# Performance work log

Hardware: AMD Instinct MI355X
Metric: run time of the kernel (lower is better)

## Reference

```python
import jax, jax.numpy as jnp
import numpy as np

D_MODEL = 384
D_INNER = 768   # expand=2
D_STATE = 16
DT_RANK = 24    # ceil(d_model/16)
D_CONV = 4
VOCAB = 50257
AUDIO_DIM = 80
B, L_AUDIO, L_TEXT = 2, 1024, 1024


def _conv1d(x, w, b, pad_l, pad_r, groups=1):
    # x: [B, C, L], w: [O, I/groups, K]
    y = jax.lax.conv_general_dilated(
        x, w, window_strides=(1,), padding=[(pad_l, pad_r)],
        feature_group_count=groups, dimension_numbers=('NCH', 'OIH', 'NCH'))
    return y + b[None, :, None]


def _mamba(x, in_w, convw, convb, xproj_w, dt_w, dt_b, A_log, Dp, out_w):
    # x: [B, L, D_MODEL]
    Bn, L, _ = x.shape
    xz = x @ in_w.T                       # [B, L, 2*D_INNER]
    xi, z = jnp.split(xz, 2, axis=-1)
    # causal depthwise conv (torch pads d_conv-1 both sides then slices [:L])
    xi = _conv1d(xi.transpose(0, 2, 1), convw, convb, D_CONV - 1, 0, groups=D_INNER)
    xi = jax.nn.silu(xi.transpose(0, 2, 1))          # [B, L, D_INNER]
    xdbl = xi @ xproj_w.T                            # [B, L, DT_RANK+2*D_STATE]
    dt, Bm, Cm = jnp.split(xdbl, [DT_RANK, DT_RANK + D_STATE], axis=-1)
    dt = jax.nn.softplus(dt @ dt_w.T + dt_b)         # [B, L, D_INNER]
    A = -jnp.exp(A_log)                              # [D_INNER, D_STATE]
    dA = jnp.exp(dt[..., None] * A)                  # [B, L, D_INNER, D_STATE]
    dBu = dt[..., None] * Bm[:, :, None, :] * xi[..., None]

    def step(h, inputs):
        dA_t, dBu_t, C_t = inputs
        h = dA_t * h + dBu_t                         # [B, D_INNER, D_STATE]
        y = jnp.einsum('bdn,bn->bd', h, C_t)
        return h, y

    h0 = jnp.zeros((Bn, D_INNER, D_STATE), dtype=x.dtype)
    _, ys = jax.lax.scan(step, h0,
                         (dA.transpose(1, 0, 2, 3), dBu.transpose(1, 0, 2, 3), Cm.transpose(1, 0, 2)))
    y = ys.transpose(1, 0, 2) + xi * Dp              # D skip connection
    y = y * jax.nn.silu(z)                           # gate
    return y @ out_w.T                               # [B, L, D_MODEL]


def setup_inputs() -> dict:
    key = jax.random.key(0)
    ks = jax.random.split(key, 16)

    def rn(k, shape, s=0.02):
        return jax.random.normal(k, shape, jnp.float32) * s

    inp = {}
    inp['audio_features'] = jax.random.normal(ks[0], (B, AUDIO_DIM, L_AUDIO), jnp.float32)
    inp['text_tokens'] = jax.random.randint(ks[1], (B, L_TEXT), 0, VOCAB)
    inp['conv1_w'] = rn(ks[2], (D_MODEL // 2, AUDIO_DIM, 3))
    inp['conv1_b'] = jnp.zeros((D_MODEL // 2,), jnp.float32)
    inp['conv2_w'] = rn(ks[3], (D_MODEL, D_MODEL // 2, 3))
    inp['conv2_b'] = jnp.zeros((D_MODEL,), jnp.float32)
    inp['embed'] = rn(ks[4], (VOCAB, D_MODEL))

    def mamba_params(kbase):
        kk = jax.random.split(kbase, 6)
        A = jnp.tile(jnp.arange(1, D_STATE + 1, dtype=jnp.float32), (D_INNER, 1))
        return dict(in_w=rn(kk[0], (2 * D_INNER, D_MODEL)),
                    convw=rn(kk[1], (D_INNER, 1, D_CONV)),
                    convb=jnp.zeros((D_INNER,), jnp.float32),
                    xproj_w=rn(kk[2], (DT_RANK + 2 * D_STATE, D_INNER)),
                    dt_w=rn(kk[3], (D_INNER, DT_RANK)),
                    dt_b=rn(kk[4], (D_INNER,), 0.1),
                    A_log=jnp.log(A),
                    Dp=jnp.ones((D_INNER,), jnp.float32),
                    out_w=rn(kk[5], (D_MODEL, D_INNER)))

    for i, p in enumerate([mamba_params(ks[5]), mamba_params(ks[6])], 1):
        for n, v in p.items():
            inp[f'm{i}_{n}'] = v
    inp['proj_w'] = rn(ks[7], (VOCAB, D_MODEL))
    inp['proj_b'] = jnp.zeros((VOCAB,), jnp.float32)
    return inp


def reference(audio_features, text_tokens, conv1_w, conv1_b, conv2_w, conv2_b, embed,
              m1_in_w, m1_convw, m1_convb, m1_xproj_w, m1_dt_w, m1_dt_b, m1_A_log, m1_Dp, m1_out_w,
              m2_in_w, m2_convw, m2_convb, m2_xproj_w, m2_dt_w, m2_dt_b, m2_A_log, m2_Dp, m2_out_w,
              proj_w, proj_b):
    a = jax.nn.relu(_conv1d(audio_features, conv1_w, conv1_b, 1, 1))
    a = _conv1d(a, conv2_w, conv2_b, 1, 1)
    audio_emb = a.transpose(0, 2, 1)                 # [B, L_audio, D_MODEL]
    text_emb = embed[text_tokens]                    # [B, L_text, D_MODEL]
    x = jnp.concatenate([audio_emb, text_emb], axis=1)
    x = _mamba(x, m1_in_w, m1_convw, m1_convb, m1_xproj_w, m1_dt_w, m1_dt_b, m1_A_log, m1_Dp, m1_out_w)
    x = _mamba(x, m2_in_w, m2_convw, m2_convb, m2_xproj_w, m2_dt_w, m2_dt_b, m2_A_log, m2_Dp, m2_out_w)
    return x @ proj_w.T + proj_b                     # [B, L, VOCAB]
```

## Files before the change

### kernel.cpp

```cpp
#include <hip/hip_runtime.h>

typedef unsigned short u16;
typedef __attribute__((ext_vector_type(4))) float f4;
typedef __attribute__((ext_vector_type(4))) float f32x4;
typedef __attribute__((ext_vector_type(8))) short short8;
typedef __attribute__((ext_vector_type(4))) unsigned short u16x4;

#define DEV static __device__ __forceinline__

DEV u16 f2bf(float f) {
  unsigned u = __float_as_uint(f);
  u += 0x7fffu + ((u >> 16) & 1u);
  return (u16)(u >> 16);
}
DEV float siluf(float z) { return z / (1.f + __expf(-z)); }

DEV void gload16(const u16* g, const u16* l) {
  __builtin_amdgcn_global_load_lds(
      (const __attribute__((address_space(1))) unsigned int*)(unsigned long long)g,
      (__attribute__((address_space(3))) unsigned int*)(unsigned int)(unsigned long long)l,
      16, 0, 0);
}

struct CvtArgs {
  const float* src[7];
  u16* dst[7];
  int bstart[8];
  int nq[7];
};

DEV void cvt_plain(const float* __restrict__ s, u16* __restrict__ d, int q, int nq) {
  if (q < nq) {
    f4 v = ((const f4*)s)[q];
    u16x4 o;
#pragma unroll
    for (int e = 0; e < 4; ++e) o[e] = f2bf(v[e]);
    ((u16x4*)d)[q] = o;
  }
}

__global__ void k_cvtmulti(CvtArgs a) {
  int b = blockIdx.x;
  int i = 0;
#pragma unroll
  for (int j = 1; j < 7; ++j) i += (b >= a.bstart[j]);
#pragma unroll
  for (int j = 0; j < 7; ++j) {
    if (i == j)
      cvt_plain(a.src[j], a.dst[j], (b - a.bstart[j]) * 256 + threadIdx.x, a.nq[j]);
  }
}

__global__ void k_wtrans(const float* __restrict__ in, float* __restrict__ out, int O, int I) {
  int n = O * I * 3;
  for (int g = blockIdx.x * blockDim.x + threadIdx.x; g < n; g += gridDim.x * blockDim.x) {
    int o = g / (I * 3);
    int rem = g - o * (I * 3);
    out[rem * O + o] = in[g];
  }
}

__global__ __launch_bounds__(192) void k_conv1(const float* __restrict__ audio,
    const float* __restrict__ w1t, const float* __restrict__ b1, float* __restrict__ a1t) {
  __shared__ float s[80][18];
  int bx = blockIdx.x;
  int b = bx >> 6, l0 = (bx & 63) << 4;
  int tid = threadIdx.x;
  for (int i = tid; i < 80 * 18; i += 192) {
    int ci = i / 18, dl = i - ci * 18;
    int l = l0 + dl - 1;
    s[ci][dl] = (l >= 0 && l < 1024) ? audio[(b * 80 + ci) * 1024 + l] : 0.f;
  }
  __syncthreads();
  int co = tid;
  float acc[16];
  float bias = b1[co];
#pragma unroll
  for (int i = 0; i < 16; ++i) acc[i] = bias;
  for (int ci = 0; ci < 80; ++ci) {
#pragma unroll
    for (int j = 0; j < 3; ++j) {
      float w = w1t[(ci * 3 + j) * 192 + co];
#pragma unroll
      for (int ls = 0; ls < 16; ++ls) acc[ls] = fmaf(s[ci][ls + j], w, acc[ls]);
    }
  }
#pragma unroll
  for (int ls = 0; ls < 16; ++ls) {
    float v = acc[ls] > 0.f ? acc[ls] : 0.f;
    a1t[(b * 1024 + l0 + ls) * 192 + co] = v;
  }
}

__global__ __launch_bounds__(384) void k_conv2b(const float* __restrict__ a1t,
    const float* __restrict__ w2t, const float* __restrict__ b2, u16* __restrict__ Xb) {
  __shared__ float s[10][192];
  int bx = blockIdx.x;
  int b = bx >> 7, l0 = (bx & 127) << 3;
  int tid = threadIdx.x;
  for (int i = tid; i < 10 * 192; i += 384) {
    int dl = i / 192, ci = i - dl * 192;
    int l = l0 + dl - 1;
    s[dl][ci] = (l >= 0 && l < 1024) ? a1t[(b * 1024 + l) * 192 + ci] : 0.f;
  }
  __syncthreads();
  int co = tid;
  float acc[8];
  float bias = b2[co];
#pragma unroll
  for (int i = 0; i < 8; ++i) acc[i] = bias;
  for (int ci = 0; ci < 192; ++ci) {
#pragma unroll
    for (int j = 0; j < 3; ++j) {
      float w = w2t[(ci * 3 + j) * 384 + co];
#pragma unroll
      for (int ls = 0; ls < 8; ++ls) acc[ls] = fmaf(s[ls + j][ci], w, acc[ls]);
    }
  }
#pragma unroll
  for (int ls = 0; ls < 8; ++ls)
    Xb[((size_t)(b * 2048 + l0 + ls)) * 384 + co] = f2bf(acc[ls]);
}

__global__ void k_embedb(const int* __restrict__ tok, const float* __restrict__ emb,
                         u16* __restrict__ Xb) {
  int gid = blockIdx.x * blockDim.x + threadIdx.x;
  if (gid >= 2 * 1024 * 96) return;
  int q = gid % 96;
  int rt = gid / 96;
  int b = rt >> 10, t = rt & 1023;
  int tk = tok[b * 1024 + t];
  f4 v = *(const f4*)(emb + (size_t)tk * 384 + q * 4);
  u16x4 o;
#pragma unroll
  for (int e = 0; e < 4; ++e) o[e] = f2bf(v[e]);
  *(u16x4*)(Xb + ((size_t)(b * 2048 + 1024 + t)) * 384 + q * 4) = o;
}

__global__ void k_dwconv2(const float* __restrict__ xz, const float* __restrict__ cw,
                          const float* __restrict__ cb, float* __restrict__ xif,
                          u16* __restrict__ xib) {
  int gid = blockIdx.x * blockDim.x + threadIdx.x;
  if (gid >= 4096 * 192) return;
  int d4 = gid % 192;
  int row = gid / 192;
  int b = row >> 11, l = row & 2047;
  int d = d4 * 4;
  f4 cw0 = *(const f4*)(cw + d * 4);
  f4 cw1 = *(const f4*)(cw + d * 4 + 4);
  f4 cw2 = *(const f4*)(cw + d * 4 + 8);
  f4 cw3 = *(const f4*)(cw + d * 4 + 12);
  f4 acc = *(const f4*)(cb + d);
#pragma unroll
  for (int j = 0; j < 4; ++j) {
    int lj = l - 3 + j;
    if (lj >= 0) {
      f4 v = *(const f4*)(xz + ((size_t)(b * 2048 + lj)) * 1536 + d);
      acc[0] = fmaf(v[0], cw0[j], acc[0]);
      acc[1] = fmaf(v[1], cw1[j], acc[1]);
      acc[2] = fmaf(v[2], cw2[j], acc[2]);
      acc[3] = fmaf(v[3], cw3[j], acc[3]);
    }
  }
  f4 o;
  u16x4 ob;
#pragma unroll
  for (int e = 0; e < 4; ++e) { o[e] = siluf(acc[e]); ob[e] = f2bf(o[e]); }
  *(f4*)(xif + (size_t)row * 768 + d) = o;
  *(u16x4*)(xib + (size_t)row * 768 + d) = ob;
}

template <int TILE, int BIAS, int ACT, int OUTB, int SWZ>
__global__ __launch_bounds__(256) void k_gemm2(
    const u16* __restrict__ A, int lda, const u16* __restrict__ W, int ldw,
    const float* __restrict__ bias, float* __restrict__ C, u16* __restrict__ Cb,
    int ldc, int M, int N, int K) {
  constexpr int MF = (TILE == 128) ? 4 : 2;
  constexpr int TB = TILE * 32;
  constexpr int NLD = (TILE == 128) ? 4 : 2;
  __shared__ u16 As[2][TB], Ws[2][TB];
  int bid = blockIdx.x;
  if (SWZ) {
    int nwg = gridDim.x;
    int q = nwg >> 3, r = nwg & 7;
    int xcd = bid & 7, li = bid >> 3;
    bid = (xcd < r ? xcd * (q + 1) : r * (q + 1) + (xcd - r) * q) + li;
  }
  int bm, bn;
  if (TILE == 128) { bm = (bid & 31) << 7; bn = (bid >> 5) << 7; }
  else             { bm = (bid & 63) << 6; bn = (bid >> 6) << 6; }
  int t = threadIdx.x, lane = t & 63, wave = t >> 6;
  int wm0, wn0;
  if (TILE == 128) { wm0 = (wave >> 1) << 6; wn0 = (wave & 1) << 6; }
  else             { wm0 = (wave >> 1) << 5; wn0 = (wave & 1) << 5; }
  int fr = lane & 15, fk = (lane >> 4) << 3;
  int r0 = t >> 2, sl = (t & 3) << 3;
  const u16* gA0 = A + (size_t)(bm + r0) * lda + sl;
  const u16* gA1 = gA0 + (size_t)64 * lda;
  int n0 = bn + r0;      if (n0 > N - 1) n0 = N - 1;
  int n1 = bn + r0 + 64; if (n1 > N - 1) n1 = N - 1;
  const u16* gW0 = W + (size_t)n0 * ldw + sl;
  const u16* gW1 = W + (size_t)n1 * ldw + sl;
  f32x4 acc[MF][MF] = {};
  int nk = K >> 5;
  auto stage = [&](int buf, int k0) {
    gload16(gA0 + k0, As[buf] + t * 8);
    gload16(gW0 + k0, Ws[buf] + t * 8);
    if (TILE == 128) {
      gload16(gA1 + k0, As[buf] + t * 8 + 2048);
      gload16(gW1 + k0, Ws[buf] + t * 8 + 2048);
    }
  };
  stage(0, 0);
  for (int s = 0; s < nk; ++s) {
    int cur = s & 1;
    if (s + 1 < nk) {
      stage(cur ^ 1, (s + 1) << 5);
      asm volatile("s_waitcnt vmcnt(%0)" :: "i"(NLD) : "memory");
    } else {
      asm volatile("s_waitcnt vmcnt(0)" ::: "memory");
    }
    __builtin_amdgcn_sched_barrier(0);
    __builtin_amdgcn_s_barrier();
    __builtin_amdgcn_sched_barrier(0);
    short8 af[MF], wf[MF];
#pragma unroll
    for (int mi = 0; mi < MF; ++mi) af[mi] = *(const short8*)&As[cur][(wm0 + mi * 16 + fr) * 32 + fk];
#pragma unroll
    for (int ni = 0; ni < MF; ++ni) wf[ni] = *(const short8*)&Ws[cur][(wn0 + ni * 16 + fr) * 32 + fk];
#pragma unroll
    for (int mi = 0; mi < MF; ++mi)
#pragma unroll
      for (int ni = 0; ni < MF; ++ni)
        acc[mi][ni] = __builtin_amdgcn_mfma_f32_16x16x32_bf16(af[mi], wf[ni], acc[mi][ni], 0, 0, 0);
    __builtin_amdgcn_sched_barrier(0);
    __builtin_amdgcn_s_barrier();
  }
  int frow = (lane >> 4) << 2;
#pragma unroll
  for (int ni = 0; ni < MF; ++ni) {
    int col = bn + wn0 + ni * 16 + fr;
    if (col < N) {
      float bv = BIAS ? bias[col] : 0.f;
#pragma unroll
      for (int mi = 0; mi < MF; ++mi) {
        int row = bm + wm0 + mi * 16 + frow;
#pragma unroll
        for (int rr = 0; rr < 4; ++rr) {
          float v = acc[mi][ni][rr] + bv;
          if (ACT == 1) v = (v > 20.f) ? v : log1pf(__expf(v));
          size_t o = (size_t)(row + rr) * ldc + col;
          if (OUTB == 0) C[o] = v;
          else if (OUTB == 1) Cb[o] = f2bf(v);
          else { C[o] = v; Cb[o] = f2bf(v); }
        }
      }
    }
  }
}

__global__ __launch_bounds__(256, 4) void k_gemmF(
    const u16* __restrict__ A, const u16* __restrict__ W,
    const float* __restrict__ bias, float* __restrict__ C,
    int ldc, int N) {
  __shared__ __align__(16) char smraw[40960];
  u16* As = (u16*)smraw;
  u16* Ws = (u16*)(smraw + 8192);
  float* Cs = (float*)smraw;
  int bid = blockIdx.x;
  {
    int nwg = gridDim.x;
    int q = nwg >> 3, r = nwg & 7;
    int xcd = bid & 7, li = bid >> 3;
    bid = (xcd < r ? xcd * (q + 1) : r * (q + 1) + (xcd - r) * q) + li;
  }
  int mg = bid / 1576;
  int rem = bid - mg * 1576;
  int np = rem >> 3, mi = rem & 7;
  int bm = ((mg << 3) + mi) << 6;
  int bn = np << 8;
  int t = threadIdx.x, lane = t & 63, wave = t >> 6;
  int wm0 = (wave >> 1) << 5;
  int wn0 = (wave & 1) << 7;
  int fr = lane & 15, hi = lane >> 4, fk = hi << 3;
  int r0 = t >> 2, sl = (t & 3) << 3;
  const u16* gA = A + (size_t)(bm + r0) * 384 + sl;
  int nrow[4];
#pragma unroll
  for (int i = 0; i < 4; ++i) {
    int gn = bn + r0 + i * 64;
    nrow[i] = (gn > N - 1) ? (N - 1) : gn;
  }
  const u16* gWs = W + sl;
  f32x4 acc[2][8] = {};
  auto stage = [&](int buf, int k0) {
    gload16(gA + k0, As + buf * 2048 + t * 8);
#pragma unroll
    for (int i = 0; i < 4; ++i)
      gload16(gWs + (size_t)nrow[i] * 384 + k0, Ws + buf * 8192 + t * 8 + i * 2048);
  };
  stage(0, 0);
  for (int s = 0; s < 12; ++s) {
    int cur = s & 1;
    if (s + 1 < 12) {
      stage(cur ^ 1, (s + 1) << 5);
      asm volatile("s_waitcnt vmcnt(5)" ::: "memory");
    } else {
      asm volatile("s_waitcnt vmcnt(0)" ::: "memory");
    }
    __builtin_amdgcn_sched_barrier(0);
    __builtin_amdgcn_s_barrier();
    __builtin_amdgcn_sched_barrier(0);
    short8 af[2];
#pragma unroll
    for (int mi2 = 0; mi2 < 2; ++mi2)
      af[mi2] = *(const short8*)&As[cur * 2048 + (wm0 + mi2 * 16 + fr) * 32 + fk];
#pragma unroll
    for (int ni = 0; ni < 8; ++ni) {
      short8 wf = *(const short8*)&Ws[cur * 8192 + (wn0 + ni * 16 + fr) * 32 + fk];
#pragma unroll
      for (int mi2 = 0; mi2 < 2; ++mi2)
        acc[mi2][ni] = __builtin_amdgcn_mfma_f32_16x16x32_bf16(af[mi2], wf, acc[mi2][ni], 0, 0, 0);
    }
    __builtin_amdgcn_sched_barrier(0);
    __builtin_amdgcn_s_barrier();
  }
  int cq = (t & 63) << 2;
  int gcol0 = bn + cq;
  f4 bv4;
  if (gcol0 + 3 < N) bv4 = *(const f4*)&bias[gcol0];
  else {
#pragma unroll
    for (int e = 0; e < 4; ++e) bv4[e] = (gcol0 + e < N) ? bias[gcol0 + e] : 0.f;
  }
  int frow = hi << 2;
#pragma unroll
  for (int c = 0; c < 2; ++c) {
    if (c) __syncthreads();
    if (wm0 == c * 32) {
#pragma unroll
      for (int ni = 0; ni < 8; ++ni) {
        int lc = wn0 + ni * 16 + fr;
#pragma unroll
        for (int mi2 = 0; mi2 < 2; ++mi2)
#pragma unroll
          for (int rr = 0; rr < 4; ++rr)
            Cs[(mi2 * 16 + frow + rr) * 260 + lc] = acc[mi2][ni][rr];
      }
    }
    __syncthreads();
#pragma unroll
    for (int p = 0; p < 8; ++p) {
      int lr = (p << 2) + (t >> 6);
      f4 v = *(const f4*)&Cs[lr * 260 + cq];
      v += bv4;
      float* cp = C + (size_t)(bm + c * 32 + lr) * ldc + gcol0;
      if (gcol0 + 3 < N) {
        __builtin_nontemporal_store(v, (f4*)cp);
      } else {
#pragma unroll
        for (int e = 0; e < 4; ++e)
          if (gcol0 + e < N) __builtin_nontemporal_store(v[e], cp + e);
      }
    }
  }
}

DEV int scan_ch0_w(int g, int w) { return (((g & 7) * 24) + ((g >> 3) << 2) + w) * 4; }

DEV void dt_inline(const float* __restrict__ xdbl, size_t rowbase, int lane,
                   const float* __restrict__ s_w, const float* __restrict__ s_b,
                   float (*s_dt)[4]) {
  const float* xr = xdbl + (rowbase + lane) * 56;
  f4 x0 = *(const f4*)xr,        x1 = *(const f4*)(xr + 4),  x2 = *(const f4*)(xr + 8);
  f4 x3 = *(const f4*)(xr + 12), x4 = *(const f4*)(xr + 16), x5 = *(const f4*)(xr + 20);
#pragma unroll
  for (int cc = 0; cc < 4; ++cc) {
    const float* w = s_w + cc * 24;
    float acc = s_b[cc];
#pragma unroll
    for (int q = 0; q < 4; ++q) acc = fmaf(x0[q], w[q], acc);
#pragma unroll
    for (int q = 0; q < 4; ++q) acc = fmaf(x1[q], w[4 + q], acc);
#pragma unroll
    for (int q = 0; q < 4; ++q) acc = fmaf(x2[q], w[8 + q], acc);
#pragma unroll
    for (int q = 0; q < 4; ++q) acc = fmaf(x3[q], w[12 + q], acc);
#pragma unroll
    for (int q = 0; q < 4; ++q) acc = fmaf(x4[q], w[16 + q], acc);
#pragma unroll
    for (int q = 0; q < 4; ++q) acc = fmaf(x5[q], w[20 + q], acc);
    s_dt[lane][cc] = (acc > 20.f) ? acc : log1pf(__expf(acc));
  }
}

__global__ __launch_bounds__(256) void k_scanA(
    const float* __restrict__ xdbl, const float* __restrict__ xi,
    const float* __restrict__ A_log,
    const float* __restrict__ dtw, const float* __restrict__ dtbias,
    float* __restrict__ Hloc, float* __restrict__ Sdt) {
  __shared__ float s_dt[4][64][4], s_w[4][96], s_b[4][4];
  int b = blockIdx.y, seg = blockIdx.z;
  int tid = threadIdx.x, w = tid >> 6, lane = tid & 63;
  int ch0 = scan_ch0_w(blockIdx.x, w);
  int c = lane >> 4, n = lane & 15;
  int d = ch0 + c;
  for (int i = lane; i < 96; i += 64) s_w[w][i] = dtw[ch0 * 24 + i];
  if (lane < 4) s_b[w][lane] = dtbias[ch0 + lane];
  size_t rowbase = (size_t)b * 2048 + seg * 64;
  __syncthreads();
  dt_inline(xdbl, rowbase, lane, s_w[w], s_b[w], s_dt[w]);
  __syncthreads();
  float a = -__expf(A_log[d * 16 + n]);
  float h = 0.f, sdt = 0.f;
  size_t row = rowbase;
#pragma unroll 4
  for (int i = 0; i < 64; ++i, ++row) {
    float dtv = s_dt[w][i][c];
    float xiv = xi[row * 768 + d];
    float Bv = xdbl[row * 56 + 24 + n];
    float da = __expf(dtv * a);
    h = fmaf(da, h, dtv * Bv * xiv);
    sdt += dtv;
  }
  size_t o = (((size_t)b * 32 + seg) * 768 + d) * 16 + n;
  Hloc[o] = h;
  if (n == 0) Sdt[((size_t)b * 32 + seg) * 768 + d] = sdt;
}

__global__ __launch_bounds__(256) void k_scanC(
    const float* __restrict__ xdbl, const float* __restrict__ xi,
    const float* __restrict__ xz, const float* __restrict__ A_log,
    const float* __restrict__ Dp,
    const float* __restrict__ dtw, const float* __restrict__ dtbias,
    const float* __restrict__ Hloc, const float* __restrict__ Sdt,
    u16* __restrict__ y) {
  __shared__ float s_dt[4][64][4], s_y[4][64][4], s_w[4][96], s_b[4][4];
  int b = blockIdx.y, seg = blockIdx.z;
  int tid = threadIdx.x, w = tid >> 6, lane = tid & 63;
  int ch0 = scan_ch0_w(blockIdx.x, w);
  int c = lane >> 4, n = lane & 15;
  int d = ch0 + c;
  for (int i = lane; i < 96; i += 64) s_w[w][i] = dtw[ch0 * 24 + i];
  if (lane < 4) s_b[w][lane] = dtbias[ch0 + lane];
  size_t rowbase = (size_t)b * 2048 + seg * 64;
  __syncthreads();
  dt_inline(xdbl, rowbase, lane, s_w[w], s_b[w], s_dt[w]);
  float a = -__expf(A_log[d * 16 + n]);
  float h = 0.f;
  for (int s = 0; s < seg; ++s) {
    float P = __expf(a * Sdt[((size_t)b * 32 + s) * 768 + d]);
    h = fmaf(P, h, Hloc[(((size_t)b * 32 + s) * 768 + d) * 16 + n]);
  }
  __syncthreads();
  size_t row = rowbase;
#pragma unroll 2
  for (int i = 0; i < 64; ++i, ++row) {
    float dtv = s_dt[w][i][c];
    float xiv = xi[row * 768 + d];
    float Bv = xdbl[row * 56 + 24 + n];
    float Cv = xdbl[row * 56 + 40 + n];
    float da = __expf(dtv * a);
    h = fmaf(da, h, dtv * Bv * xiv);
    float yv = h * Cv;
    yv += __shfl_xor(yv, 1);
    yv += __shfl_xor(yv, 2);
    yv += __shfl_xor(yv, 4);
    yv += __shfl_xor(yv, 8);
    if (n == 0) s_y[w][i][c] = yv;
  }
  __syncthreads();
  size_t rw = rowbase + lane;
  f4 xiv4 = *(const f4*)(xi + rw * 768 + ch0);
  f4 dpv = *(const f4*)(Dp + ch0);
  f4 zv = *(const f4*)(xz + rw * 1536 + 768 + ch0);
  u16x4 ob;
#pragma unroll
  for (int e = 0; e < 4; ++e) {
    float o = (s_y[w][lane][e] + xiv4[e] * dpv[e]) * siluf(zv[e]);
    ob[e] = f2bf(o);
  }
  *(u16x4*)(y + rw * 768 + ch0) = ob;
}

extern "C" void kernel_launch(void* const* d_in, const int* in_sizes, int n_in,
                              void* d_out, int out_size, void* d_ws, size_t ws_size,
                              hipStream_t stream) {
  const float* audio   = (const float*)d_in[0];
  const int*   tokens  = (const int*)d_in[1];
  const float* conv1_w = (const float*)d_in[2];
  const float* conv1_b = (const float*)d_in[3];
  const float* conv2_w = (const float*)d_in[4];
  const float* conv2_b = (const float*)d_in[5];
  const float* embedw  = (const float*)d_in[6];
  const float* P1[9], *P2[9];
  for (int i = 0; i < 9; ++i) { P1[i] = (const float*)d_in[7 + i]; P2[i] = (const float*)d_in[16 + i]; }
  const float* proj_w = (const float*)d_in[25];
  const float* proj_b = (const float*)d_in[26];
  (void)in_sizes; (void)n_in; (void)out_size; (void)ws_size;

  float* base = (float*)d_out;
  size_t off = 0;
  auto af = [&](size_t n) { float* p = base + off; off += n; return p; };
  float* xz   = af((size_t)4096 * 1536);
  float* xif  = af((size_t)4096 * 768);
  float* xdbl = af((size_t)4096 * 56);
  float* a1t  = af((size_t)2 * 1024 * 192);
  float* w1t  = af((size_t)80 * 3 * 192);
  float* w2t  = af((size_t)192 * 3 * 384);
  float* Hloc = af((size_t)2 * 32 * 768 * 16);
  float* Sdt  = af((size_t)2 * 32 * 768);
  u16* ub = (u16*)(base + off);
  size_t uoff = 0;
  auto au = [&](size_t n) { u16* p = ub + uoff; uoff += n; return p; };
  u16* Xin_b  = au((size_t)4096 * 384);
  u16* Xmid_b = au((size_t)4096 * 384);
  u16* xib    = au((size_t)4096 * 768);
  u16* yb16   = au((size_t)4096 * 768);
  u16* Wi1 = au((size_t)1536 * 384);
  u16* Wx1 = au((size_t)56 * 768);
  u16* Wo1 = au((size_t)384 * 768);
  u16* Wi2 = au((size_t)1536 * 384);
  u16* Wx2 = au((size_t)56 * 768);
  u16* Wo2 = au((size_t)384 * 768);
  u16* X2b    = (u16*)d_ws;
  u16* projwb = X2b + (size_t)4096 * 384;

  CvtArgs ca;
  const float* srcs[7] = {P1[0], P1[3], P1[8], P2[0], P2[3], P2[8], proj_w};
  u16* dsts[7] = {Wi1, Wx1, Wo1, Wi2, Wx2, Wo2, projwb};
  int nqs[7] = {147456, 10752, 73728, 147456, 10752, 73728, 4824672};
  int cum = 0;
  for (int j = 0; j < 7; ++j) {
    ca.src[j] = srcs[j]; ca.dst[j] = dsts[j]; ca.nq[j] = nqs[j];
    ca.bstart[j] = cum; cum += (nqs[j] + 255) / 256;
  }
  ca.bstart[7] = cum;
  k_cvtmulti<<<dim3(cum), dim3(256), 0, stream>>>(ca);

  k_wtrans<<<dim3(180), dim3(256), 0, stream>>>(conv1_w, w1t, 192, 80);
  k_wtrans<<<dim3(864), dim3(256), 0, stream>>>(conv2_w, w2t, 384, 192);
  k_conv1<<<dim3(128), dim3(192), 0, stream>>>(audio, w1t, conv1_b, a1t);
  k_conv2b<<<dim3(256), dim3(384), 0, stream>>>(a1t, w2t, conv2_b, Xin_b);
  k_embedb<<<dim3(768), dim3(256), 0, stream>>>(tokens, embedw, Xin_b);

  auto run_mamba = [&](const float* const* P, const u16* Xin, u16* Xout,
                       const u16* Wi, const u16* Wx, const u16* Wo) {
    k_gemm2<64, 0, 0, 0, 1><<<dim3(64 * 24), dim3(256), 0, stream>>>(
        Xin, 384, Wi, 384, nullptr, xz, nullptr, 1536, 4096, 1536, 384);
    k_dwconv2<<<dim3(3072), dim3(256), 0, stream>>>(xz, P[1], P[2], xif, xib);
    k_gemm2<64, 0, 0, 0, 0><<<dim3(64 * 1), dim3(256), 0, stream>>>(
        xib, 768, Wx, 768, nullptr, xdbl, nullptr, 56, 4096, 56, 768);
    k_scanA<<<dim3(48, 2, 32), dim3(256), 0, stream>>>(
        xdbl, xif, P[6], P[4], P[5], Hloc, Sdt);
    k_scanC<<<dim3(48, 2, 32), dim3(256), 0, stream>>>(
        xdbl, xif, xz, P[6], P[7], P[4], P[5], Hloc, Sdt, yb16);
    k_gemm2<64, 0, 0, 1, 0><<<dim3(64 * 6), dim3(256), 0, stream>>>(
        yb16, 768, Wo, 768, nullptr, nullptr, Xout, 384, 4096, 384, 768);
  };
  run_mamba(P1, Xin_b, Xmid_b, Wi1, Wx1, Wo1);
  run_mamba(P2, Xmid_b, X2b, Wi2, Wx2, Wo2);

  k_gemmF<<<dim3(64 * 197), dim3(256), 0, stream>>>(
      X2b, projwb, proj_b, (float*)d_out, 50257, 50257);
}
```

Measured before the change: 625.6 us.

## Fuse depthwise conv+SiLU with x_proj GEMM via in-register MFMA

Replaces the separate depthwise-conv kernel and the 56-column x_proj GEMM with one kernel. Each block handles 16 rows, computes conv+SiLU, writes the fp32 activations, and feeds bf16 fragments straight into MFMA against Wx. Four warps split K and are reduced through shared memory. This removes the bf16 intermediate buffer round trip and a launch, and replaces the old 64-block GEMM with 256 blocks. In exchange, xz loads become per-row strided and Wx is re-read from global by every block.

```diff
diff --git a/kernel.cpp b/kernel.cpp
--- a/kernel.cpp
+++ b/kernel.cpp
@@ -137,37 +137,71 @@
   *(u16x4*)(Xb + ((size_t)(b * 2048 + 1024 + t)) * 384 + q * 4) = o;
 }
 
-__global__ void k_dwconv2(const float* __restrict__ xz, const float* __restrict__ cw,
-                          const float* __restrict__ cb, float* __restrict__ xif,
-                          u16* __restrict__ xib) {
-  int gid = blockIdx.x * blockDim.x + threadIdx.x;
-  if (gid >= 4096 * 192) return;
-  int d4 = gid % 192;
-  int row = gid / 192;
-  int b = row >> 11, l = row & 2047;
-  int d = d4 * 4;
-  f4 cw0 = *(const f4*)(cw + d * 4);
-  f4 cw1 = *(const f4*)(cw + d * 4 + 4);
-  f4 cw2 = *(const f4*)(cw + d * 4 + 8);
-  f4 cw3 = *(const f4*)(cw + d * 4 + 12);
-  f4 acc = *(const f4*)(cb + d);
-#pragma unroll
-  for (int j = 0; j < 4; ++j) {
-    int lj = l - 3 + j;
-    if (lj >= 0) {
-      f4 v = *(const f4*)(xz + ((size_t)(b * 2048 + lj)) * 1536 + d);
-      acc[0] = fmaf(v[0], cw0[j], acc[0]);
-      acc[1] = fmaf(v[1], cw1[j], acc[1]);
-      acc[2] = fmaf(v[2], cw2[j], acc[2]);
-      acc[3] = fmaf(v[3], cw3[j], acc[3]);
-    }
-  }
-  f4 o;
-  u16x4 ob;
-#pragma unroll
-  for (int e = 0; e < 4; ++e) { o[e] = siluf(acc[e]); ob[e] = f2bf(o[e]); }
-  *(f4*)(xif + (size_t)row * 768 + d) = o;
-  *(u16x4*)(xib + (size_t)row * 768 + d) = ob;
+__global__ __launch_bounds__(256) void k_dwx(
+    const float* __restrict__ xz, const float* __restrict__ cw,
+    const float* __restrict__ cb, const u16* __restrict__ Wx,
+    float* __restrict__ xif, float* __restrict__ xdbl) {
+  __shared__ float s_cw[3072], s_cb[768];
+  __shared__ float part[4][16][64];
+  int t = threadIdx.x, w = t >> 6, lane = t & 63;
+  int fr = lane & 15, hi = lane >> 4;
+  for (int i = t; i < 3072; i += 256) s_cw[i] = cw[i];
+  for (int i = t; i < 768; i += 256) s_cb[i] = cb[i];
+  int r0 = blockIdx.x << 4;
+  int r = r0 + fr;
+  int l = r & 2047;
+  __syncthreads();
+  f32x4 acc[4] = {};
+  for (int c = 0; c < 6; ++c) {
+    int ch = w * 192 + c * 32 + hi * 8;
+    float v[8];
+#pragma unroll
+    for (int e = 0; e < 8; ++e) v[e] = s_cb[ch + e];
+#pragma unroll
+    for (int j = 0; j < 4; ++j) {
+      if (l - 3 + j >= 0) {
+        const float* xp = xz + (size_t)(r - 3 + j) * 1536 + ch;
+        f4 a0 = *(const f4*)xp, a1 = *(const f4*)(xp + 4);
+#pragma unroll
+        for (int e = 0; e < 4; ++e) {
+          v[e]     = fmaf(a0[e], s_cw[(ch + e) * 4 + j], v[e]);
+          v[4 + e] = fmaf(a1[e], s_cw[(ch + 4 + e) * 4 + j], v[4 + e]);
+        }
+      }
+    }
+    short8 af;
+    f4 o0, o1;
+#pragma unroll
+    for (int e = 0; e < 4; ++e) {
+      float s0 = siluf(v[e]), s1 = siluf(v[4 + e]);
+      o0[e] = s0; o1[e] = s1;
+      af[e] = (short)f2bf(s0); af[4 + e] = (short)f2bf(s1);
+    }
+    *(f4*)(xif + (size_t)r * 768 + ch) = o0;
+    *(f4*)(xif + (size_t)r * 768 + ch + 4) = o1;
+#pragma unroll
+    for (int nf = 0; nf < 4; ++nf) {
+      int col = nf * 16 + fr;
+      int wr = (col < 56) ? col : 55;
+      short8 wf = *(const short8*)(Wx + (size_t)wr * 768 + ch);
+      acc[nf] = __builtin_amdgcn_mfma_f32_16x16x32_bf16(af, wf, acc[nf], 0, 0, 0);
+    }
+  }
+#pragma unroll
+  for (int nf = 0; nf < 4; ++nf)
+#pragma unroll
+    for (int rr = 0; rr < 4; ++rr)
+      part[w][hi * 4 + rr][nf * 16 + fr] = acc[nf][rr];
+  __syncthreads();
+#pragma unroll
+  for (int kk = 0; kk < 4; ++kk) {
+    int idx = t * 4 + kk;
+    int rr = idx >> 6, cc = idx & 63;
+    if (cc < 56) {
+      float s = part[0][rr][cc] + part[1][rr][cc] + part[2][rr][cc] + part[3][rr][cc];
+      xdbl[(size_t)(r0 + rr) * 56 + cc] = s;
+    }
+  }
 }
 
 template <int TILE, int BIAS, int ACT, int OUTB, int SWZ>
@@ -515,7 +549,6 @@
   auto au = [&](size_t n) { u16* p = ub + uoff; uoff += n; return p; };
   u16* Xin_b  = au((size_t)4096 * 384);
   u16* Xmid_b = au((size_t)4096 * 384);
-  u16* xib    = au((size_t)4096 * 768);
   u16* yb16   = au((size_t)4096 * 768);
   u16* Wi1 = au((size_t)1536 * 384);
   u16* Wx1 = au((size_t)56 * 768);
@@ -548,9 +581,7 @@
                        const u16* Wi, const u16* Wx, const u16* Wo) {
     k_gemm2<64, 0, 0, 0, 1><<<dim3(64 * 24), dim3(256), 0, stream>>>(
         Xin, 384, Wi, 384, nullptr, xz, nullptr, 1536, 4096, 1536, 384);
-    k_dwconv2<<<dim3(3072), dim3(256), 0, stream>>>(xz, P[1], P[2], xif, xib);
-    k_gemm2<64, 0, 0, 0, 0><<<dim3(64 * 1), dim3(256), 0, stream>>>(
-        xib, 768, Wx, 768, nullptr, xdbl, nullptr, 56, 4096, 56, 768);
+    k_dwx<<<dim3(256), dim3(256), 0, stream>>>(xz, P[1], P[2], Wx, xif, xdbl);
     k_scanA<<<dim3(48, 2, 32), dim3(256), 0, stream>>>(
         xdbl, xif, P[6], P[4], P[5], Hloc, Sdt);
     k_scanC<<<dim3(48, 2, 32), dim3(256), 0, stream>>>(
```

After: 628.0 us. No clear change (+0.4%).
